# Optimization experiments

Measured on AMD Instinct MI355X. Metric: run time of the kernel, lower is better.

The kernel has to match this reference:

```python
import jax, jax.numpy as jnp
import numpy as np
from jax import lax

D_MODEL = 64
D_STATE = 16
D_INNER = 128   # expand * d_model
DT_RANK = 4     # ceil(d_model / 16)
D_CONV = 4      # mamba_ssm default causal conv width
N_MAMBA = 6


def _gelu(x):
    return jax.nn.gelu(x, approximate=False)


def _conv2d(x, w, b, groups=1):
    ph, pw = w.shape[2] // 2, w.shape[3] // 2
    y = lax.conv_general_dilated(x, w, (1, 1), [(ph, ph), (pw, pw)],
                                 dimension_numbers=('NCHW', 'OIHW', 'NCHW'),
                                 feature_group_count=groups)
    return y + b[None, :, None, None]


def _group_norm(x, w, b, groups=4, eps=1e-5):
    B, C, H, W = x.shape
    xr = x.reshape(B, groups, C // groups, H * W)
    m = xr.mean((2, 3), keepdims=True)
    v = ((xr - m) ** 2).mean((2, 3), keepdims=True)
    xr = (xr - m) * lax.rsqrt(v + eps)
    return xr.reshape(B, C, H, W) * w[None, :, None, None] + b[None, :, None, None]


def _res_conv(x, p):
    c1w, c1b, g1w, g1b, c2w, c2b, g2w, g2b = p
    h = _gelu(_group_norm(_conv2d(x, c1w, c1b), g1w, g1b))
    h = _group_norm(_conv2d(h, c2w, c2b), g2w, g2b)
    return _gelu(x + h)


def _mamba(u, in_w, conv_w, conv_b, xproj_w, dt_w, dt_b, A_log, Dp, out_w):
    # u: (B, L, d_model). Standard Mamba-1 selective scan via parallel assoc scan.
    x, z = jnp.split(u @ in_w.T, 2, axis=-1)            # (B,L,Di) each
    # causal depthwise conv1d, kernel D_CONV
    xt = lax.conv_general_dilated(x.transpose(0, 2, 1), conv_w[:, None, :], (1,),
                                  [(D_CONV - 1, 0)],
                                  dimension_numbers=('NCH', 'OIH', 'NCH'),
                                  feature_group_count=D_INNER)
    x = jax.nn.silu((xt + conv_b[None, :, None]).transpose(0, 2, 1))
    dt, Bc, Cc = jnp.split(x @ xproj_w.T, [DT_RANK, DT_RANK + D_STATE], axis=-1)
    dt = jax.nn.softplus(dt @ dt_w.T + dt_b)            # (B,L,Di)
    A = -jnp.exp(A_log)                                  # (Di,N)
    dA = jnp.exp(dt[..., None] * A)                      # (B,L,Di,N)
    dBx = dt[..., None] * Bc[:, :, None, :] * x[..., None]

    def comb(e1, e2):  # h_t = a_t*h_{t-1} + b_t
        a1, b1 = e1
        a2, b2 = e2
        return a1 * a2, b1 * a2 + b2

    _, h = lax.associative_scan(comb, (dA, dBx), axis=1)  # (B,L,Di,N)
    y = jnp.einsum('blds,bls->bld', h, Cc) + Dp * x
    y = y * jax.nn.silu(z)
    return y @ out_w.T


def _bi_mamba(u, mp, i_fwd, i_bwd):
    f = _mamba(u, *[p[i_fwd] for p in mp])
    b = jnp.flip(_mamba(jnp.flip(u, 1), *[p[i_bwd] for p in mp]), 1)
    return 0.5 * (f + b)


def _forward(x, m_in_w, m_conv_w, m_conv_b, m_xproj_w, m_dt_w, m_dt_b, m_A_log,
             m_D, m_out_w, r1_c1_w, r1_c1_b, r1_g1_w, r1_g1_b, r1_c2_w, r1_c2_b,
             r1_g2_w, r1_g2_b, dw_w, dw_b, pw_w, pw_b, r2_c1_w, r2_c1_b, r2_g1_w,
             r2_g1_b, r2_c2_w, r2_c2_b, r2_g2_w, r2_g2_b):
    B, D, H, W = x.shape
    mp = (m_in_w, m_conv_w, m_conv_b, m_xproj_w, m_dt_w, m_dt_b, m_A_log, m_D, m_out_w)
    x_flat = x.reshape(B, D, H * W).transpose(0, 2, 1)   # (B, HW, D)
    # spatial bidirectional mamba
    x_spatial = _bi_mamba(x_flat, mp, 0, 1).transpose(0, 2, 1).reshape(B, D, H, W)
    # local conv branch
    xl = _res_conv(x_spatial, (r1_c1_w, r1_c1_b, r1_g1_w, r1_g1_b, r1_c2_w, r1_c2_b, r1_g2_w, r1_g2_b))
    xl = _gelu(_conv2d(xl, dw_w, dw_b, groups=D))
    xl = _conv2d(xl, pw_w, pw_b)
    xl = _res_conv(xl, (r2_c1_w, r2_c1_b, r2_g1_w, r2_g1_b, r2_c2_w, r2_c2_b, r2_g2_w, r2_g2_b))
    # 'time' branch on original input (same flattening as x_flat)
    x_tg = _bi_mamba(x_flat, mp, 2, 3).transpose(0, 2, 1).reshape(B, D, H, W)
    # downsampled branch
    x_ds = x.reshape(B, D, H // 2, 2, W // 2, 2).mean((3, 5))
    ds_flat = x_ds.reshape(B, D, (H // 2) * (W // 2)).transpose(0, 2, 1)
    x_td = _bi_mamba(ds_flat, mp, 4, 5).transpose(0, 2, 1).reshape(B, D, H // 2, W // 2)
    x_td = jax.image.resize(x_td, (B, D, H, W), method='bilinear')
    return x_spatial + xl + 0.5 * x_tg + 0.5 * x_td


def setup_inputs() -> dict:
    key = jax.random.key(0)
    ks = iter(jax.random.split(key, 64))

    def rn(shape, s=0.02):
        return (s * jax.random.normal(next(ks), shape)).astype(jnp.float32)

    D, Di, N, R = D_MODEL, D_INNER, D_STATE, DT_RANK
    inp = {
        'x': jax.random.normal(next(ks), (2, D, 64, 64), dtype=jnp.float32),
        'm_in_w': rn((N_MAMBA, 2 * Di, D)),
        'm_conv_w': rn((N_MAMBA, Di, D_CONV), 0.1),
        'm_conv_b': rn((N_MAMBA, Di), 0.1),
        'm_xproj_w': rn((N_MAMBA, R + 2 * N, Di)),
        'm_dt_w': rn((N_MAMBA, Di, R), 0.1),
        'm_dt_b': rn((N_MAMBA, Di), 0.5),
        'm_A_log': jnp.tile(jnp.log(jnp.arange(1, N + 1, dtype=jnp.float32)), (N_MAMBA, Di, 1)),
        'm_D': jnp.ones((N_MAMBA, Di), jnp.float32),
        'm_out_w': rn((N_MAMBA, D, Di)),
        'dw_w': rn((D, 1, 3, 3), 0.1), 'dw_b': rn((D,), 0.1),
        'pw_w': rn((D, D, 1, 1), 0.05), 'pw_b': rn((D,), 0.1),
    }
    for pre in ('r1', 'r2'):
        inp[pre + '_c1_w'] = rn((D, D, 3, 3), 0.05)
        inp[pre + '_c1_b'] = rn((D,), 0.1)
        inp[pre + '_g1_w'] = jnp.ones((D,), jnp.float32)
        inp[pre + '_g1_b'] = jnp.zeros((D,), jnp.float32)
        inp[pre + '_c2_w'] = rn((D, D, 3, 3), 0.05)
        inp[pre + '_c2_b'] = rn((D,), 0.1)
        inp[pre + '_g2_w'] = jnp.ones((D,), jnp.float32)
        inp[pre + '_g2_b'] = jnp.zeros((D,), jnp.float32)
    return inp


def reference(x, m_in_w, m_conv_w, m_conv_b, m_xproj_w, m_dt_w, m_dt_b, m_A_log,
              m_D, m_out_w, r1_c1_w, r1_c1_b, r1_g1_w, r1_g1_b, r1_c2_w, r1_c2_b,
              r1_g2_w, r1_g2_b, dw_w, dw_b, pw_w, pw_b, r2_c1_w, r2_c1_b, r2_g1_w,
              r2_g1_b, r2_c2_w, r2_c2_b, r2_g2_w, r2_g2_b):
    return _forward(x, m_in_w, m_conv_w, m_conv_b, m_xproj_w, m_dt_w, m_dt_b,
                    m_A_log, m_D, m_out_w, r1_c1_w, r1_c1_b, r1_g1_w, r1_g1_b,
                    r1_c2_w, r1_c2_b, r1_g2_w, r1_g2_b, dw_w, dw_b, pw_w, pw_b,
                    r2_c1_w, r2_c1_b, r2_g1_w, r2_g1_b, r2_c2_w, r2_c2_b,
                    r2_g2_w, r2_g2_b)
```

## Files before the change

kernel.cpp:

```cpp
#include <hip/hip_runtime.h>
#include <hip/hip_bf16.h>

typedef __hip_bfloat16 bf16;
typedef unsigned short u16;
typedef unsigned int u32;
typedef __attribute__((ext_vector_type(8))) short short8v;
typedef __attribute__((ext_vector_type(4))) float f32x4;


#define XCB_OFF   0u
#define DTB_OFF   2359296u
#define BCB_OFF   4718592u
#define CHA_OFF   5308416u
#define CHH_OFF   7667712u
#define XZ_OFF    10027008u
#define UFS_OFF   14745600u
#define UFD_OFF   15269888u
#define XS_OFF    15400960u
#define XTG_OFF   15925248u
#define XTD_OFF   16449536u
#define XSB_OFF   16580608u
#define WT4_OFF   16842752u
#define STATS_OFF 16916480u
#define FLAG_OFF  16916736u
#define PRM_OFF   16916752u
#define PART_OFF  17091184u
#define CV0_OFF   0u
#define CV1_OFF   524288u
#define A1B_OFF   1048576u
#define A2B_OFF   1310720u
#define PWB_OFF   1572864u

__device__ __forceinline__ float bits2f(u16 v){
  u32 u = ((u32)v) << 16; float f; __builtin_memcpy(&f, &u, 4); return f;
}
__device__ __forceinline__ float b2f(bf16 v){ return __bfloat162float(v); }
__device__ __forceinline__ u16 f2bu(float f){ bf16 h = __float2bfloat16(f); u16 b; __builtin_memcpy(&b, &h, 2); return b; }
__device__ __forceinline__ float silu_f(float x){ return x / (1.f + __expf(-x)); }
__device__ __forceinline__ float softplus_f(float x){ return fmaxf(x, 0.f) + log1pf(__expf(-fabsf(x))); }
__device__ __forceinline__ float gelu_f(float x){ return 0.5f * x * (1.f + erff(x * 0.70710678118654752f)); }
__device__ __forceinline__ short8v zero8(){ short8v z = {0,0,0,0,0,0,0,0}; return z; }
__device__ __forceinline__ void up2(u32 w, float& a, float& b){
  a = bits2f((u16)(w & 0xffffu)); b = bits2f((u16)(w >> 16));
}
__device__ __forceinline__ void powchain(float r, float* aa){
  aa[0]=r; aa[1]=r*r; aa[2]=aa[1]*r; aa[3]=aa[1]*aa[1];
  aa[4]=aa[3]*r; aa[5]=aa[3]*aa[1]; aa[6]=aa[3]*aa[2]; aa[7]=aa[3]*aa[3];
  aa[8]=aa[7]*r; aa[9]=aa[7]*aa[1]; aa[10]=aa[7]*aa[2]; aa[11]=aa[7]*aa[3];
  aa[12]=aa[7]*aa[4]; aa[13]=aa[7]*aa[5]; aa[14]=aa[7]*aa[6]; aa[15]=aa[7]*aa[7];
}

struct P29 { const void* p[29]; };

__constant__ int PREF[30] = {0, 98304, 101376, 102144, 129792, 132864, 133632,
  145920, 146688, 195840, 196416, 196480, 200576, 200640, 237504, 237568,
  237632, 237696, 274560, 274624, 274688, 274752, 311616, 311680, 311744,
  311808, 348672, 348736, 348800, 348864};

__constant__ float LOGT[16] = {0.0f, 0.6931472f, 1.0986123f, 1.3862944f,
  1.6094379f, 1.7917595f, 1.9459101f, 2.0794415f, 2.1972246f, 2.3025851f,
  2.3978953f, 2.4849067f, 2.5649493f, 2.6390573f, 2.7080502f, 2.7725887f};

__global__ void k_detect(const void* __restrict__ xraw, const void* __restrict__ araw,
                         float* __restrict__ ws){
  __shared__ int cnt_s, bad_s;
  int tid = threadIdx.x;
  if (tid == 0){ cnt_s = 0; bad_s = 0; }
  __syncthreads();
  const u16* p = (const u16*)xraw;
  int c = 0;
  for (int i = tid; i < 4096; i += 256){
    int e = (p[i] >> 7) & 0xFF;
    if (e >= 0x77 && e <= 0x87) c++;
  }
  atomicAdd(&cnt_s, c);
  __syncthreads();
  int flag = (cnt_s > 3500) ? 0 : 1;
  int bad = 0;
  for (int i = tid; i < 12288; i += 256){
    float v = flag ? ((const float*)araw)[i] : b2f(((const bf16*)araw)[i]);
    if (fabsf(v - LOGT[i & 15]) > 0.02f) bad = 1;
  }
  if (bad) atomicAdd(&bad_s, 1);
  __syncthreads();
  if (tid == 0){
    ((int*)(ws + FLAG_OFF))[0] = flag;
    ((int*)(ws + FLAG_OFF))[1] = (bad_s == 0) ? 1 : 0;
  }
}

__global__ __launch_bounds__(256) void k_setup(P29 ptrs, const void* __restrict__ xraw,
                                               float* __restrict__ ws){
  int bid = blockIdx.x, tid = threadIdx.x;
  int flag = *(const int*)(ws + FLAG_OFF);
  const float* xf = (const float*)xraw;
  const bf16*  xb = (const bf16*)xraw;
  if (bid < 2560){
    int i = bid * 256 + tid;
    if (i < 524288){
      int b = i >> 18, rem = i & 262143, l = rem >> 6, d = rem & 63;
      size_t idx = (size_t)b*262144 + d*4096 + l;
      ws[UFS_OFF + i] = flag ? xf[idx] : b2f(xb[idx]);
    } else if (i < 655360){
      int j = i - 524288;
      int b = j >> 16, rem = j & 65535, l = rem >> 6, d = rem & 63;
      int i2 = l >> 5, j2 = l & 31;
      size_t base = (size_t)b*262144 + d*4096 + (i2*2)*64 + j2*2;
      float v0, v1, v2, v3;
      if (flag){ v0 = xf[base]; v1 = xf[base+1]; v2 = xf[base+64]; v3 = xf[base+65]; }
      else     { v0 = b2f(xb[base]); v1 = b2f(xb[base+1]); v2 = b2f(xb[base+64]); v3 = b2f(xb[base+65]); }
      ws[UFD_OFF + j] = 0.25f * (v0 + v1 + v2 + v3);
    }
  } else if (bid < 3923){
    int i = (bid - 2560) * 256 + tid;
    if (i < 348864){
      int t = 0;
      #pragma unroll 1
      while (i >= PREF[t + 1]) ++t;
      int off = i - PREF[t];
      float v = flag ? ((const float*)ptrs.p[t])[off]
                     : b2f(((const bf16*)ptrs.p[t])[off]);
      ((bf16*)(ws + PRM_OFF))[i] = __float2bfloat16(v);
    }
  } else {
    int i = (bid - 3923) * 256 + tid;
    if (i < 147456){
      int conv = i / 36864, r = i - conv * 36864;
      int tap = r >> 12, co = (r >> 6) & 63, ci = r & 63;
      const int SRC[4] = {13, 17, 21, 25};
      const void* sp_ = ptrs.p[SRC[conv]];
      size_t off = (size_t)co * 576 + ci * 9 + tap;
      float v = flag ? ((const float*)sp_)[off] : b2f(((const bf16*)sp_)[off]);
      ((bf16*)(ws + WT4_OFF))[i] = __float2bfloat16(v);
    }
  }
}

__device__ __forceinline__ void chunk_map(int bid, int& g, int& c0){
  if (bid < 1024){ g = bid >> 7; c0 = bid & 127; }
  else { int r = bid - 1024; g = 8 + (r >> 5); c0 = r & 31; }
}

__global__ __launch_bounds__(256) void k_inproj(const float* __restrict__ ws,
        bf16* __restrict__ XZ, const bf16* __restrict__ in_w){
  __shared__ __align__(16) u16 u_s[32][72];
  int g, tile; chunk_map(blockIdx.x, g, tile);
  int dir = (g < 8) ? (g >> 1) : 4 + ((g - 8) >> 1);
  int b   = (g < 8) ? (g & 1) : ((g - 8) & 1);
  int rev = dir & 1;
  int L   = (g < 8) ? 4096 : 1024;
  int row0 = (g < 8) ? g * 4096 : 32768 + (g - 8) * 1024;
  int t0 = tile * 32;
  const float* U = (g < 8) ? (ws + UFS_OFF + (size_t)b * 262144)
                           : (ws + UFD_OFF + (size_t)b * 65536);
  int tid = threadIdx.x;
  for (int e = tid; e < 2048; e += 256){
    int i = e >> 6, d = e & 63;
    int l = rev ? (L - 1 - (t0 + i)) : (t0 + i);
    u_s[i][d] = f2bu(U[(size_t)l * 64 + d]);
  }
  __syncthreads();
  int w = tid >> 6, lane = tid & 63;
  int l15 = lane & 15, ko = lane >> 4;
  short8v Au[2][2];
  #pragma unroll
  for (int mt = 0; mt < 2; ++mt)
    #pragma unroll
    for (int kk = 0; kk < 2; ++kk)
      Au[mt][kk] = *(const short8v*)&u_s[mt * 16 + l15][kk * 32 + ko * 8];
  const u16* wg = (const u16*)in_w + (size_t)dir * 16384;
  u16* XZu = (u16*)XZ;
  #pragma unroll
  for (int nq = 0; nq < 4; ++nq){
    int nt = w * 4 + nq;
    int c = nt * 16 + l15;
    short8v B0 = *(const short8v*)(wg + (size_t)c * 64 + ko * 8);
    short8v B1 = *(const short8v*)(wg + (size_t)c * 64 + 32 + ko * 8);
    #pragma unroll
    for (int mt = 0; mt < 2; ++mt){
      f32x4 acc = {0.f, 0.f, 0.f, 0.f};
      acc = __builtin_amdgcn_mfma_f32_16x16x32_bf16(Au[mt][0], B0, acc, 0, 0, 0);
      acc = __builtin_amdgcn_mfma_f32_16x16x32_bf16(Au[mt][1], B1, acc, 0, 0, 0);
      #pragma unroll
      for (int reg = 0; reg < 4; ++reg){
        int t = t0 + mt * 16 + ko * 4 + reg;
        XZu[(size_t)(row0 + t) * 256 + c] = f2bu(acc[reg]);
      }
    }
  }
}

__global__ __launch_bounds__(256) void k_front(float* __restrict__ ws,
        const bf16* __restrict__ xproj_w, const bf16* __restrict__ dt_w, const bf16* __restrict__ dt_b,
        const bf16* __restrict__ conv_w, const bf16* __restrict__ conv_b, const bf16* __restrict__ A_log){
  __shared__ __align__(16) u32 xstage[2310];
  __shared__ __align__(16) u16 xc_s[32][136];
  __shared__ __align__(16) u32 blob[4352];
  float* xp_s = (float*)xstage;
  u16* xw_s = (u16*)blob;
  float* cmb = (float*)blob;

  int g, c0; chunk_map(blockIdx.x, g, c0);
  int dir = (g < 8) ? (g >> 1) : 4 + ((g - 8) >> 1);
  int grow0 = (g < 8) ? g * 4096 : 32768 + (g - 8) * 1024;
  int t0 = c0 << 5;
  int crow = ((g < 8) ? g * 128 : 1024 + (g - 8) * 32) + c0;
  int tid = threadIdx.x;

  const u32* XZ32 = (const u32*)(ws + XZ_OFF);
  for (int e = tid; e < 2240; e += 256){
    int lr = e >> 6, col = e & 63;
    int gt = t0 - 3 + lr;
    u32 v = 0u;
    if (gt >= 0) v = XZ32[(size_t)(grow0 + gt) * 128 + col];
    xstage[lr * 66 + col] = v;
  }
  const u16* xw = (const u16*)xproj_w + (size_t)dir * 4608;
  for (int e = tid; e < 6144; e += 256){
    int m = e >> 7, col = e & 127;
    xw_s[m * 136 + col] = (m < 36) ? xw[m * 128 + col] : (u16)0;
  }
  __syncthreads();

  int c = tid & 127, hf = tid >> 7;
  int rb = hf * 16;
  {
    const u16* cwp = (const u16*)conv_w + (size_t)dir * 512 + c * 4;
    uint2 cw2 = *(const uint2*)cwp;
    float cw0, cw1, cw2f, cw3;
    up2(cw2.x, cw0, cw1); up2(cw2.y, cw2f, cw3);
    float cb = b2f(conv_b[dir * 128 + c]);
    const u16* xsu = (const u16*)xstage;
    float xm3 = bits2f(xsu[rb * 132 + c]);
    float xm2 = bits2f(xsu[(rb + 1) * 132 + c]);
    float xm1 = bits2f(xsu[(rb + 2) * 132 + c]);
    u16* XCBu = (u16*)(ws + XCB_OFF);
    #pragma unroll 4
    for (int t = 0; t < 16; ++t){
      float xcur = bits2f(xsu[(rb + t + 3) * 132 + c]);
      float s = cb + cw0 * xm3 + cw1 * xm2 + cw2f * xm1 + cw3 * xcur;
      u16 xbv = f2bu(silu_f(s));
      xm3 = xm2; xm2 = xm1; xm1 = xcur;
      xc_s[rb + t][c] = xbv;
      XCBu[(size_t)(grow0 + t0 + rb + t) * 128 + c] = xbv;
    }
  }
  __syncthreads();

  {
    int w = tid >> 6, lane = tid & 63;
    int l15 = lane & 15, ko = lane >> 4;
    for (int task = w; task < 6; task += 4){
      int mt = task & 1, nt = task >> 1;
      f32x4 acc = {0.f, 0.f, 0.f, 0.f};
      #pragma unroll
      for (int kk = 0; kk < 4; ++kk){
        short8v Afr = *(const short8v*)&xc_s[mt * 16 + l15][kk * 32 + ko * 8];
        short8v Bfr = *(const short8v*)(xw_s + (size_t)(nt * 16 + l15) * 136 + kk * 32 + ko * 8);
        acc = __builtin_amdgcn_mfma_f32_16x16x32_bf16(Afr, Bfr, acc, 0, 0, 0);
      }
      int j = nt * 16 + l15;
      if (j < 36){
        #pragma unroll
        for (int reg = 0; reg < 4; ++reg){
          int t = mt * 16 + ko * 4 + reg;
          xp_s[t * 40 + j] = acc[reg];
        }
      }
    }
  }
  __syncthreads();

  {
    u16* BCBu = (u16*)(ws + BCB_OFF);
    for (int e = tid; e < 1024; e += 256){
      int t = e >> 5, v = e & 31;
      float val = xp_s[t * 40 + 4 + v];
      u16 r = f2bu(val);
      xp_s[t * 40 + 4 + v] = bits2f(r);
      BCBu[(size_t)(grow0 + t0 + t) * 32 + v] = r;
    }
  }
  __syncthreads();

  {
    int apat = ((const int*)(ws + FLAG_OFF))[1];
    float A[16];
    const u16* ap = (const u16*)A_log + (size_t)dir * 2048 + c * 16;
    #pragma unroll
    for (int s = 0; s < 16; ++s) A[s] = -__expf(bits2f(ap[s]));
    const u16* dwp = (const u16*)dt_w + (size_t)dir * 512 + c * 4;
    uint2 dw2 = *(const uint2*)dwp;
    float d0, d1, d2, d3;
    up2(dw2.x, d0, d1); up2(dw2.y, d2, d3);
    float db = b2f(dt_b[dir * 128 + c]);
    u16* DTBu = (u16*)(ws + DTB_OFF);
    float hh[16], p[16];
    #pragma unroll
    for (int s = 0; s < 16; ++s){ hh[s] = 0.f; p[s] = 1.f; }
    float dtsum = 0.f;
    #pragma unroll 2
    for (int t = 0; t < 16; ++t){
      float4 xp4 = *(const float4*)&xp_s[(rb + t) * 40];
      float dtv = softplus_f(db + d0 * xp4.x + d1 * xp4.y + d2 * xp4.z + d3 * xp4.w);
      u16 dtb16 = f2bu(dtv);
      DTBu[(size_t)(grow0 + t0 + rb + t) * 128 + c] = dtb16;
      float dtu = bits2f(dtb16);
      float xcv = bits2f(xc_s[rb + t][c]);
      float dx = dtu * xcv;
      float aa[16];
      if (apat){
        dtsum += dtu;
        powchain(__expf(-dtu), aa);
      } else {
        #pragma unroll
        for (int s = 0; s < 16; ++s) aa[s] = __expf(dtu * A[s]);
        #pragma unroll
        for (int s = 0; s < 16; ++s) p[s] *= aa[s];
      }
      #pragma unroll
      for (int s = 0; s < 16; ++s)
        hh[s] = fmaf(aa[s], hh[s], dx * xp_s[(rb + t) * 40 + 4 + s]);
    }
    if (apat) powchain(__expf(-dtsum), p);
    if (hf == 0){
      #pragma unroll
      for (int s = 0; s < 16; ++s){
        cmb[c * 17 + s] = p[s];
        cmb[2176 + c * 17 + s] = hh[s];
      }
    }
    __syncthreads();
    if (hf == 1){
      float ca[16], ch[16];
      #pragma unroll
      for (int s = 0; s < 16; ++s){
        float P0 = cmb[c * 17 + s];
        float H0 = cmb[2176 + c * 17 + s];
        ca[s] = P0 * p[s];
        ch[s] = fmaf(p[s], H0, hh[s]);
      }
      float* CA = ws + CHA_OFF + (size_t)crow * 2048 + c * 16;
      float* CH = ws + CHH_OFF + (size_t)crow * 2048 + c * 16;
      #pragma unroll
      for (int q = 0; q < 4; ++q){
        *(float4*)(CA + q * 4) = make_float4(ca[q*4], ca[q*4+1], ca[q*4+2], ca[q*4+3]);
        *(float4*)(CH + q * 4) = make_float4(ch[q*4], ch[q*4+1], ch[q*4+2], ch[q*4+3]);
      }
    }
  }
}

__global__ __launch_bounds__(256) void k_scan2(float* __restrict__ ws){
  int id = blockIdx.x * 256 + threadIdx.x;
  int gi = id >> 11, dsl = id & 2047;
  int nc = (gi < 8) ? 128 : 32;
  int cb = (gi < 8) ? gi * 128 : 1024 + (gi - 8) * 32;
  float* CA = ws + CHA_OFF; float* CH = ws + CHH_OFF;
  float hprev = 0.f;
  for (int ch = 0; ch < nc; ch += 8){
    size_t i0 = (size_t)(cb + ch) * 2048 + dsl;
    float a[8], hv[8];
    #pragma unroll
    for (int j = 0; j < 8; ++j){
      a[j] = CA[i0 + (size_t)j * 2048];
      hv[j] = CH[i0 + (size_t)j * 2048];
    }
    #pragma unroll
    for (int j = 0; j < 8; ++j){
      CH[i0 + (size_t)j * 2048] = hprev;
      hprev = fmaf(a[j], hprev, hv[j]);
    }
  }
}

__global__ __launch_bounds__(256) void k_outproj(float* __restrict__ ws, const bf16* __restrict__ out_w,
        const bf16* __restrict__ A_log, const bf16* __restrict__ Dp){
  __shared__ __align__(16) u16 yf_s[32][132];
  __shared__ __align__(16) u16 yb_s[32][132];
  int bid = blockIdx.x;
  int pair, b, tile, L;
  if (bid < 512){ pair = bid >> 8; b = (bid >> 7) & 1; tile = bid & 127; L = 4096; }
  else { int r = bid - 512; pair = 2; b = r >> 5; tile = r & 31; L = 1024; }
  int l0 = tile * 32;
  int ncht = L >> 5;
  int df = pair * 2, db_ = df + 1;
  int gf = (pair < 2) ? df * 2 + b : 8 + b;
  int gb = (pair < 2) ? db_ * 2 + b : 10 + b;
  int rowf0 = (gf < 8) ? gf * 4096 : 32768 + (gf - 8) * 1024;
  int rowb0 = (gb < 8) ? gb * 4096 : 32768 + (gb - 8) * 1024;
  int tid = threadIdx.x;

  {
    int half = tid >> 7, d = tid & 127;
    int gS = half ? gb : gf;
    int dirS = (gS < 8) ? (gS >> 1) : 4 + ((gS - 8) >> 1);
    int rowS = half ? (rowb0 + (L - 32 - l0)) : (rowf0 + l0);
    int cbaseS = (gS < 8) ? gS * 128 : 1024 + (gS - 8) * 32;
    int crowS = cbaseS + (half ? (ncht - 1 - tile) : tile);
    int apat = ((const int*)(ws + FLAG_OFF))[1];
    float A[16];
    const u16* ap = (const u16*)A_log + (size_t)dirS * 2048 + d * 16;
    #pragma unroll
    for (int s = 0; s < 16; ++s) A[s] = -__expf(bits2f(ap[s]));
    float h[16];
    const float* CH = ws + CHH_OFF + (size_t)crowS * 2048 + d * 16;
    #pragma unroll
    for (int s = 0; s < 16; ++s) h[s] = CH[s];
    float Dv = b2f(Dp[dirS * 128 + d]);
    const u16* XCBu = (const u16*)(ws + XCB_OFF);
    const u16* DTBu = (const u16*)(ws + DTB_OFF);
    const u16* BCBu = (const u16*)(ws + BCB_OFF);
    const u16* XZu  = (const u16*)(ws + XZ_OFF);
    #pragma unroll 2
    for (int t = 0; t < 32; ++t){
      size_t r = (size_t)(rowS + t);
      float dtu = bits2f(DTBu[r * 128 + d]);
      float xcv = bits2f(XCBu[r * 128 + d]);
      float zv  = bits2f(XZu[r * 256 + 128 + d]);
      const uint4* bp = (const uint4*)(BCBu + r * 32);
      uint4 q0 = bp[0], q1 = bp[1], q2 = bp[2], q3 = bp[3];
      float Bv[16], Cv[16];
      up2(q0.x, Bv[0], Bv[1]);  up2(q0.y, Bv[2], Bv[3]);  up2(q0.z, Bv[4], Bv[5]);  up2(q0.w, Bv[6], Bv[7]);
      up2(q1.x, Bv[8], Bv[9]);  up2(q1.y, Bv[10], Bv[11]); up2(q1.z, Bv[12], Bv[13]); up2(q1.w, Bv[14], Bv[15]);
      up2(q2.x, Cv[0], Cv[1]);  up2(q2.y, Cv[2], Cv[3]);  up2(q2.z, Cv[4], Cv[5]);  up2(q2.w, Cv[6], Cv[7]);
      up2(q3.x, Cv[8], Cv[9]);  up2(q3.y, Cv[10], Cv[11]); up2(q3.z, Cv[12], Cv[13]); up2(q3.w, Cv[14], Cv[15]);
      float dx = dtu * xcv;
      float aa[16];
      if (apat){
        powchain(__expf(-dtu), aa);
      } else {
        #pragma unroll
        for (int s = 0; s < 16; ++s) aa[s] = __expf(dtu * A[s]);
      }
      float y = 0.f;
      #pragma unroll
      for (int s = 0; s < 16; ++s){
        h[s] = fmaf(aa[s], h[s], dx * Bv[s]);
        y = fmaf(h[s], Cv[s], y);
      }
      y = fmaf(Dv, xcv, y);
      u16 yv = f2bu(y * silu_f(zv));
      if (half == 0) yf_s[t][d] = yv;
      else           yb_s[31 - t][d] = yv;
    }
  }
  __syncthreads();

  int w = tid >> 6, lane = tid & 63;
  int l15 = lane & 15, ko = lane >> 4;
  int mt = w & 1, nh = w >> 1;
  const u16* wf = (const u16*)out_w + (size_t)df * 8192;
  const u16* wb = (const u16*)out_w + (size_t)db_ * 8192;
  short8v Af[4], Ab[4];
  #pragma unroll
  for (int kk = 0; kk < 4; ++kk){
    Af[kk] = *(const short8v*)&yf_s[mt * 16 + l15][kk * 32 + ko * 8];
    Ab[kk] = *(const short8v*)&yb_s[mt * 16 + l15][kk * 32 + ko * 8];
  }
  float* xo = ws + ((pair == 0) ? XS_OFF : (pair == 1) ? XTG_OFF : XTD_OFF);
  int Lout = (pair < 2) ? 4096 : 1024;
  u16* xsb = (u16*)(ws + XSB_OFF);
  #pragma unroll
  for (int ct = 0; ct < 2; ++ct){
    int c = nh * 32 + ct * 16 + l15;
    f32x4 acc = {0.f, 0.f, 0.f, 0.f};
    #pragma unroll
    for (int kk = 0; kk < 4; ++kk){
      short8v Bf = *(const short8v*)(wf + (size_t)c * 128 + kk * 32 + ko * 8);
      acc = __builtin_amdgcn_mfma_f32_16x16x32_bf16(Af[kk], Bf, acc, 0, 0, 0);
      short8v Bb = *(const short8v*)(wb + (size_t)c * 128 + kk * 32 + ko * 8);
      acc = __builtin_amdgcn_mfma_f32_16x16x32_bf16(Ab[kk], Bb, acc, 0, 0, 0);
    }
    #pragma unroll
    for (int reg = 0; reg < 4; ++reg){
      int row = l0 + mt * 16 + ko * 4 + reg;
      float v = 0.5f * acc[reg];
      xo[((size_t)b * Lout + row) * 64 + c] = v;
      if (pair == 0) xsb[((size_t)b * 4096 + row) * 64 + c] = f2bu(v);
    }
  }
}

template<int NTAP>
__global__ __launch_bounds__(256) void k_convmfma(const bf16* __restrict__ act,
        float* __restrict__ outf, bf16* __restrict__ outb,
        const bf16* __restrict__ wt, const bf16* __restrict__ bias,
        float* __restrict__ part){
  __shared__ float red[4][4];
  int wid = blockIdx.x * 4 + (threadIdx.x >> 6);
  int lane = threadIdx.x & 63;
  int nc = wid & 1;
  int pt = wid >> 1;
  int b = pt >> 8, py = (pt >> 2) & 63, x0 = (pt & 3) << 4;
  int l15 = lane & 15, ko = lane >> 4;
  f32x4 acc0 = {0.f, 0.f, 0.f, 0.f}, acc1 = {0.f, 0.f, 0.f, 0.f};
  const bf16* ab = act + ((size_t)b * 4096) * 64;
  #pragma unroll
  for (int tap = 0; tap < NTAP; ++tap){
    int dy = (NTAP == 9) ? (tap / 3 - 1) : 0;
    int dx = (NTAP == 9) ? (tap % 3 - 1) : 0;
    int y = py + dy;
    bool yok = (NTAP == 1) || ((unsigned)y < 64u);
    int xx = x0 + l15 + dx;
    bool vall = yok && ((NTAP == 1) || ((unsigned)xx < 64u));
    const bf16* arow = ab + ((size_t)(y * 64 + xx)) * 64;
    const bf16* wrow = wt + (size_t)tap * 4096;
    #pragma unroll
    for (int kk = 0; kk < 2; ++kk){
      int ci0 = kk * 32 + ko * 8;
      short8v a;
      if (vall) a = *(const short8v*)(arow + ci0); else a = zero8();
      short8v bw0 = *(const short8v*)(wrow + (size_t)(nc * 32 + l15) * 64 + ci0);
      short8v bw1 = *(const short8v*)(wrow + (size_t)(nc * 32 + 16 + l15) * 64 + ci0);
      acc0 = __builtin_amdgcn_mfma_f32_16x16x32_bf16(a, bw0, acc0, 0, 0, 0);
      acc1 = __builtin_amdgcn_mfma_f32_16x16x32_bf16(a, bw1, acc1, 0, 0, 0);
    }
  }
  float bs0 = b2f(bias[nc * 32 + l15]);
  float bs1 = b2f(bias[nc * 32 + 16 + l15]);
  float s1a = 0.f, s2a = 0.f, s1b = 0.f, s2b = 0.f;
  size_t obase = ((size_t)b * 4096 + py * 64 + x0 + (ko << 2)) * 64 + nc * 32;
  #pragma unroll
  for (int r = 0; r < 4; ++r){
    float v0 = acc0[r] + bs0, v1 = acc1[r] + bs1;
    s1a += v0; s2a += v0 * v0; s1b += v1; s2b += v1 * v1;
    if (outf){
      outf[obase + (size_t)r * 64 + l15] = v0;
      outf[obase + (size_t)r * 64 + 16 + l15] = v1;
    } else {
      outb[obase + (size_t)r * 64 + l15] = __float2bfloat16(v0);
      outb[obase + (size_t)r * 64 + 16 + l15] = __float2bfloat16(v1);
    }
  }
  #pragma unroll
  for (int off = 1; off < 64; off <<= 1){
    s1a += __shfl_xor(s1a, off, 64); s2a += __shfl_xor(s2a, off, 64);
    s1b += __shfl_xor(s1b, off, 64); s2b += __shfl_xor(s2b, off, 64);
  }
  int w = threadIdx.x >> 6;
  if (lane == 0){ red[w][0] = s1a; red[w][1] = s2a; red[w][2] = s1b; red[w][3] = s2b; }
  __syncthreads();
  if (part && threadIdx.x < 8){
    int g = threadIdx.x >> 1, sel = threadIdx.x & 1;
    int w0 = g >> 1;
    int col = ((g & 1) << 1) + sel;
    part[(size_t)blockIdx.x * 8 + threadIdx.x] = red[w0][col] + red[w0 + 2][col];
  }
}

__global__ __launch_bounds__(256) void k_gn_act(const float* __restrict__ in, const float* __restrict__ res,
        bf16* __restrict__ outb, const float* __restrict__ part,
        const bf16* __restrict__ gw, const bf16* __restrict__ gb, int add_res){
  __shared__ float st8[8];
  int tid = threadIdx.x;
  int t = blockIdx.x * 256 + tid;
  int b = blockIdx.x >> 8;
  {
    int j = tid & 31, f = tid >> 5;
    float v = 0.f;
    #pragma unroll
    for (int k = 0; k < 4; ++k)
      v += part[(size_t)(b * 128 + j * 4 + k) * 8 + f];
    #pragma unroll
    for (int off = 16; off; off >>= 1) v += __shfl_down(v, off, 32);
    if (j == 0) st8[f] = v;
  }
  __syncthreads();
  int cq = t & 15, px = (t >> 4) & 4095;
  int c0 = cq * 4, g = cq >> 2;
  float mean = st8[g * 2] * (1.f / 65536.f);
  float rs = rsqrtf(st8[g * 2 + 1] * (1.f / 65536.f) - mean * mean + 1e-5f);
  size_t idx = ((size_t)b * 4096 + px) * 64 + c0;
  float4 f4 = *(const float4*)(in + idx);
  float vv[4] = {f4.x, f4.y, f4.z, f4.w};
  float rr[4] = {0.f, 0.f, 0.f, 0.f};
  if (add_res){ float4 r4 = *(const float4*)(res + idx); rr[0]=r4.x; rr[1]=r4.y; rr[2]=r4.z; rr[3]=r4.w; }
  u16 o[4];
  #pragma unroll
  for (int j = 0; j < 4; ++j){
    float v = (vv[j] - mean) * rs * b2f(gw[c0 + j]) + b2f(gb[c0 + j]);
    v += rr[j];
    o[j] = f2bu(gelu_f(v));
  }
  u32 lo = (u32)o[0] | ((u32)o[1] << 16);
  u32 hi = (u32)o[2] | ((u32)o[3] << 16);
  *(uint2*)((u16*)outb + idx) = make_uint2(lo, hi);
}

__global__ __launch_bounds__(256) void k_dwgelu(const bf16* __restrict__ in, bf16* __restrict__ out,
        const bf16* __restrict__ w, const bf16* __restrict__ bias){
  int id = blockIdx.x * 256 + threadIdx.x;
  int oc8 = id & 7, px = (id >> 3) & 4095, b = id >> 15;
  int py = px >> 6, pxx = px & 63;
  float wv[8][9];
  #pragma unroll
  for (int j = 0; j < 8; ++j)
    #pragma unroll
    for (int tp = 0; tp < 9; ++tp) wv[j][tp] = b2f(w[(oc8 * 8 + j) * 9 + tp]);
  float acc[8];
  #pragma unroll
  for (int j = 0; j < 8; ++j) acc[j] = b2f(bias[oc8 * 8 + j]);
  const bf16* inb = in + ((size_t)b * 4096) * 64;
  #pragma unroll
  for (int dy = 0; dy < 3; ++dy){
    int y = py + dy - 1;
    if ((unsigned)y >= 64u) continue;
    #pragma unroll
    for (int dx = 0; dx < 3; ++dx){
      int x = pxx + dx - 1;
      if ((unsigned)x >= 64u) continue;
      short8v iv = *(const short8v*)(inb + ((size_t)(y * 64 + x)) * 64 + oc8 * 8);
      #pragma unroll
      for (int j = 0; j < 8; ++j)
        acc[j] = fmaf(bits2f((u16)iv[j]), wv[j][dy * 3 + dx], acc[j]);
    }
  }
  u32 pk[4];
  #pragma unroll
  for (int k = 0; k < 4; ++k){
    u16 a0 = f2bu(gelu_f(acc[2 * k]));
    u16 a1 = f2bu(gelu_f(acc[2 * k + 1]));
    pk[k] = (u32)a0 | ((u32)a1 << 16);
  }
  *(uint4*)((u16*)out + ((size_t)b * 4096 + px) * 64 + oc8 * 8) = make_uint4(pk[0], pk[1], pk[2], pk[3]);
}

__global__ __launch_bounds__(256) void k_final(const float* __restrict__ ws, void* __restrict__ outp,
        const bf16* __restrict__ gw, const bf16* __restrict__ gb){
  __shared__ float st8[8];
  int flag = *(const int*)(ws + FLAG_OFF);
  int bid = blockIdx.x;
  int b = bid >> 6, py = bid & 63;
  int t = threadIdx.x;
  {
    const float* part = ws + PART_OFF + 3 * 2048;
    int j = t & 31, f = t >> 5;
    float v = 0.f;
    #pragma unroll
    for (int k = 0; k < 4; ++k)
      v += part[(size_t)(b * 128 + j * 4 + k) * 8 + f];
    #pragma unroll
    for (int off = 16; off; off >>= 1) v += __shfl_down(v, off, 32);
    if (j == 0) st8[f] = v;
  }
  __syncthreads();
  int c = t & 63, pxg = t >> 6;
  int g = c >> 4;
  float mean = st8[g * 2] * (1.f / 65536.f);
  float rs = rsqrtf(st8[g * 2 + 1] * (1.f / 65536.f) - mean * mean + 1e-5f);
  float gwv = b2f(gw[c]), gbv = b2f(gb[c]);
  const float* CV1 = ws + CV1_OFF;
  const bf16* PWB = (const bf16*)(ws + PWB_OFF);
  const float* XS = ws + XS_OFF;
  const float* XTG = ws + XTG_OFF;
  const float* XTD = ws + XTD_OFF + ((size_t)b * 1024) * 64;
  float sy = 0.5f * py - 0.25f;
  float fly = floorf(sy); float fy = sy - fly;
  int iy0 = max((int)fly, 0), iy1 = min((int)fly + 1, 31);
  float of[16];
  #pragma unroll
  for (int i = 0; i < 16; ++i){
    int px = pxg * 16 + i;
    size_t idx = ((size_t)b * 4096 + py * 64 + px) * 64 + c;
    float gn = (CV1[idx] - mean) * rs * gwv + gbv;
    float xl = gelu_f(b2f(PWB[idx]) + gn);
    float sx = 0.5f * px - 0.25f;
    float flx = floorf(sx); float fx = sx - flx;
    int ix0 = max((int)flx, 0), ix1 = min((int)flx + 1, 31);
    float v00 = XTD[(size_t)(iy0 * 32 + ix0) * 64 + c], v01 = XTD[(size_t)(iy0 * 32 + ix1) * 64 + c];
    float v10 = XTD[(size_t)(iy1 * 32 + ix0) * 64 + c], v11 = XTD[(size_t)(iy1 * 32 + ix1) * 64 + c];
    float tdv = (1.f - fy) * ((1.f - fx) * v00 + fx * v01) + fy * ((1.f - fx) * v10 + fx * v11);
    of[i] = XS[idx] + xl + 0.5f * XTG[idx] + 0.5f * tdv;
  }
  size_t ob = ((size_t)(b * 64 + c)) * 4096 + py * 64 + pxg * 16;
  if (flag){
    float* o = (float*)outp + ob;
    #pragma unroll
    for (int k = 0; k < 4; ++k)
      *(float4*)(o + k * 4) = make_float4(of[k*4], of[k*4+1], of[k*4+2], of[k*4+3]);
  } else {
    u16* o = (u16*)outp + ob;
    u32 pk[8];
    #pragma unroll
    for (int k = 0; k < 8; ++k)
      pk[k] = (u32)f2bu(of[2*k]) | ((u32)f2bu(of[2*k+1]) << 16);
    *(uint4*)(o) = make_uint4(pk[0], pk[1], pk[2], pk[3]);
    *(uint4*)(o + 8) = make_uint4(pk[4], pk[5], pk[6], pk[7]);
  }
}

extern "C" void kernel_launch(void* const* d_in, const int* in_sizes, int n_in,
                              void* d_out, int out_size, void* d_ws, size_t ws_size,
                              hipStream_t stream) {
  float* ws = (float*)d_ws;
  bf16* XZ = (bf16*)(ws + XZ_OFF);
  bf16* prm = (bf16*)(ws + PRM_OFF);
  bf16* WT4 = (bf16*)(ws + WT4_OFF);
  bf16* XSB = (bf16*)(ws + XSB_OFF);
  bf16* A1B = (bf16*)(ws + A1B_OFF);
  bf16* A2B = (bf16*)(ws + A2B_OFF);
  bf16* PWBb = (bf16*)(ws + PWB_OFF);
  float* CV0 = ws + CV0_OFF;
  float* CV1 = ws + CV1_OFF;
  float* PART = ws + PART_OFF;

  const bf16* m_in_w   = prm + 0;
  const bf16* m_conv_w = prm + 98304;
  const bf16* m_conv_b = prm + 101376;
  const bf16* m_xproj  = prm + 102144;
  const bf16* m_dt_w   = prm + 129792;
  const bf16* m_dt_b   = prm + 132864;
  const bf16* m_A_log  = prm + 133632;
  const bf16* m_D      = prm + 145920;
  const bf16* m_out_w  = prm + 146688;
  const bf16* dw_w  = prm + 195840;
  const bf16* dw_b  = prm + 196416;
  const bf16* pw_w  = prm + 196480;
  const bf16* pw_b  = prm + 200576;
  const bf16* r1c1b = prm + 237504;
  const bf16* r1g1w = prm + 237568;
  const bf16* r1g1b = prm + 237632;
  const bf16* r1c2b = prm + 274560;
  const bf16* r1g2w = prm + 274624;
  const bf16* r1g2b = prm + 274688;
  const bf16* r2c1b = prm + 311616;
  const bf16* r2g1w = prm + 311680;
  const bf16* r2g1b = prm + 311744;
  const bf16* r2c2b = prm + 348672;
  const bf16* r2g2w = prm + 348736;
  const bf16* r2g2b = prm + 348800;

  P29 ptrs;
  for (int t = 0; t < 29; ++t) ptrs.p[t] = d_in[t + 1];

  k_detect<<<1, 256, 0, stream>>>(d_in[0], d_in[7], ws);
  k_setup<<<4499, 256, 0, stream>>>(ptrs, d_in[0], ws);
  k_inproj<<<1152, 256, 0, stream>>>(ws, XZ, m_in_w);
  k_front<<<1152, 256, 0, stream>>>(ws, m_xproj, m_dt_w, m_dt_b, m_conv_w, m_conv_b, m_A_log);
  k_scan2<<<96, 256, 0, stream>>>(ws);
  k_outproj<<<576, 256, 0, stream>>>(ws, m_out_w, m_A_log, m_D);

  k_convmfma<9><<<256, 256, 0, stream>>>(XSB, CV0, (bf16*)nullptr, WT4 + 0 * 36864, r1c1b, PART + 0 * 2048);
  k_gn_act<<<512, 256, 0, stream>>>(CV0, (const float*)nullptr, A1B, PART + 0 * 2048, r1g1w, r1g1b, 0);
  k_convmfma<9><<<256, 256, 0, stream>>>(A1B, CV1, (bf16*)nullptr, WT4 + 1 * 36864, r1c2b, PART + 1 * 2048);
  k_gn_act<<<512, 256, 0, stream>>>(CV1, ws + XS_OFF, A2B, PART + 1 * 2048, r1g2w, r1g2b, 1);
  k_dwgelu<<<256, 256, 0, stream>>>(A2B, A1B, dw_w, dw_b);
  k_convmfma<1><<<256, 256, 0, stream>>>(A1B, (float*)nullptr, PWBb, pw_w, pw_b, (float*)nullptr);
  k_convmfma<9><<<256, 256, 0, stream>>>(PWBb, CV0, (bf16*)nullptr, WT4 + 2 * 36864, r2c1b, PART + 2 * 2048);
  k_gn_act<<<512, 256, 0, stream>>>(CV0, (const float*)nullptr, A1B, PART + 2 * 2048, r2g1w, r2g1b, 0);
  k_convmfma<9><<<256, 256, 0, stream>>>(A1B, CV1, (bf16*)nullptr, WT4 + 3 * 36864, r2c2b, PART + 3 * 2048);
  k_final<<<128, 256, 0, stream>>>(ws, d_out, r2g2w, r2g2b);
}
```

Baseline: 206.8 us.

## Fuse Mamba input projection into front kernel, recomputing conv halo rows

Merges the in_proj MFMA kernel into k_front so the x half of the projection stays in shared memory instead of being written to and re-read from global XZ. Only the z half is still stored globally. The three causal-conv halo rows before each 32-row chunk are recomputed per block with scalar FMAs from the input. This removes one kernel launch and a global round trip of the x activations, at the cost of redundant halo work, more shared memory per block and extra scalar FMAs.

```diff
diff --git a/kernel.cpp b/kernel.cpp
--- a/kernel.cpp
+++ b/kernel.cpp
@@ -141,84 +141,94 @@
   else { int r = bid - 1024; g = 8 + (r >> 5); c0 = r & 31; }
 }
 
-__global__ __launch_bounds__(256) void k_inproj(const float* __restrict__ ws,
-        bf16* __restrict__ XZ, const bf16* __restrict__ in_w){
-  __shared__ __align__(16) u16 u_s[32][72];
-  int g, tile; chunk_map(blockIdx.x, g, tile);
+__global__ __launch_bounds__(256) void k_front(float* __restrict__ ws, const bf16* __restrict__ in_w,
+        const bf16* __restrict__ xproj_w, const bf16* __restrict__ dt_w, const bf16* __restrict__ dt_b,
+        const bf16* __restrict__ conv_w, const bf16* __restrict__ conv_b, const bf16* __restrict__ A_log){
+  __shared__ __align__(16) u32 pool[1280];
+  __shared__ __align__(16) u16 x_s[35 * 132];
+  __shared__ __align__(16) u16 xc_s[32][136];
+  __shared__ __align__(16) u32 blob[4352];
+  u16* u_s = (u16*)pool;
+  float* xp_s = (float*)pool;
+  u16* xw_s = (u16*)blob;
+  float* cmb = (float*)blob;
+
+  int g, c0; chunk_map(blockIdx.x, g, c0);
   int dir = (g < 8) ? (g >> 1) : 4 + ((g - 8) >> 1);
-  int b   = (g < 8) ? (g & 1) : ((g - 8) & 1);
+  int bb  = (g < 8) ? (g & 1) : ((g - 8) & 1);
   int rev = dir & 1;
   int L   = (g < 8) ? 4096 : 1024;
-  int row0 = (g < 8) ? g * 4096 : 32768 + (g - 8) * 1024;
-  int t0 = tile * 32;
-  const float* U = (g < 8) ? (ws + UFS_OFF + (size_t)b * 262144)
-                           : (ws + UFD_OFF + (size_t)b * 65536);
-  int tid = threadIdx.x;
-  for (int e = tid; e < 2048; e += 256){
-    int i = e >> 6, d = e & 63;
-    int l = rev ? (L - 1 - (t0 + i)) : (t0 + i);
-    u_s[i][d] = f2bu(U[(size_t)l * 64 + d]);
-  }
-  __syncthreads();
-  int w = tid >> 6, lane = tid & 63;
-  int l15 = lane & 15, ko = lane >> 4;
-  short8v Au[2][2];
-  #pragma unroll
-  for (int mt = 0; mt < 2; ++mt)
-    #pragma unroll
-    for (int kk = 0; kk < 2; ++kk)
-      Au[mt][kk] = *(const short8v*)&u_s[mt * 16 + l15][kk * 32 + ko * 8];
-  const u16* wg = (const u16*)in_w + (size_t)dir * 16384;
-  u16* XZu = (u16*)XZ;
-  #pragma unroll
-  for (int nq = 0; nq < 4; ++nq){
-    int nt = w * 4 + nq;
-    int c = nt * 16 + l15;
-    short8v B0 = *(const short8v*)(wg + (size_t)c * 64 + ko * 8);
-    short8v B1 = *(const short8v*)(wg + (size_t)c * 64 + 32 + ko * 8);
-    #pragma unroll
-    for (int mt = 0; mt < 2; ++mt){
-      f32x4 acc = {0.f, 0.f, 0.f, 0.f};
-      acc = __builtin_amdgcn_mfma_f32_16x16x32_bf16(Au[mt][0], B0, acc, 0, 0, 0);
-      acc = __builtin_amdgcn_mfma_f32_16x16x32_bf16(Au[mt][1], B1, acc, 0, 0, 0);
-      #pragma unroll
-      for (int reg = 0; reg < 4; ++reg){
-        int t = t0 + mt * 16 + ko * 4 + reg;
-        XZu[(size_t)(row0 + t) * 256 + c] = f2bu(acc[reg]);
-      }
-    }
-  }
-}
-
-__global__ __launch_bounds__(256) void k_front(float* __restrict__ ws,
-        const bf16* __restrict__ xproj_w, const bf16* __restrict__ dt_w, const bf16* __restrict__ dt_b,
-        const bf16* __restrict__ conv_w, const bf16* __restrict__ conv_b, const bf16* __restrict__ A_log){
-  __shared__ __align__(16) u32 xstage[2310];
-  __shared__ __align__(16) u16 xc_s[32][136];
-  __shared__ __align__(16) u32 blob[4352];
-  float* xp_s = (float*)xstage;
-  u16* xw_s = (u16*)blob;
-  float* cmb = (float*)blob;
-
-  int g, c0; chunk_map(blockIdx.x, g, c0);
-  int dir = (g < 8) ? (g >> 1) : 4 + ((g - 8) >> 1);
   int grow0 = (g < 8) ? g * 4096 : 32768 + (g - 8) * 1024;
   int t0 = c0 << 5;
   int crow = ((g < 8) ? g * 128 : 1024 + (g - 8) * 32) + c0;
+  const float* U = (g < 8) ? (ws + UFS_OFF + (size_t)bb * 262144)
+                           : (ws + UFD_OFF + (size_t)bb * 65536);
   int tid = threadIdx.x;
 
-  const u32* XZ32 = (const u32*)(ws + XZ_OFF);
   for (int e = tid; e < 2240; e += 256){
-    int lr = e >> 6, col = e & 63;
+    int lr = e >> 6, k = e & 63;
     int gt = t0 - 3 + lr;
-    u32 v = 0u;
-    if (gt >= 0) v = XZ32[(size_t)(grow0 + gt) * 128 + col];
-    xstage[lr * 66 + col] = v;
+    float v = 0.f;
+    if (gt >= 0){
+      int l = rev ? (L - 1 - gt) : gt;
+      v = U[(size_t)l * 64 + k];
+    }
+    u_s[lr * 72 + k] = f2bu(v);
   }
   const u16* xw = (const u16*)xproj_w + (size_t)dir * 4608;
   for (int e = tid; e < 6144; e += 256){
     int m = e >> 7, col = e & 127;
     xw_s[m * 136 + col] = (m < 36) ? xw[m * 128 + col] : (u16)0;
+  }
+  __syncthreads();
+
+  {
+    int w = tid >> 6, lane = tid & 63;
+    int l15 = lane & 15, ko = lane >> 4;
+    short8v Au[2][2];
+    #pragma unroll
+    for (int mt = 0; mt < 2; ++mt)
+      #pragma unroll
+      for (int kk = 0; kk < 2; ++kk)
+        Au[mt][kk] = *(const short8v*)(u_s + (size_t)(3 + mt * 16 + l15) * 72 + kk * 32 + ko * 8);
+    const u16* wg = (const u16*)in_w + (size_t)dir * 16384;
+    u16* XZu = (u16*)(ws + XZ_OFF);
+    #pragma unroll
+    for (int nq = 0; nq < 4; ++nq){
+      int nt = w * 4 + nq;
+      int c = nt * 16 + l15;
+      short8v B0 = *(const short8v*)(wg + (size_t)c * 64 + ko * 8);
+      short8v B1 = *(const short8v*)(wg + (size_t)c * 64 + 32 + ko * 8);
+      #pragma unroll
+      for (int mt = 0; mt < 2; ++mt){
+        f32x4 acc = {0.f, 0.f, 0.f, 0.f};
+        acc = __builtin_amdgcn_mfma_f32_16x16x32_bf16(Au[mt][0], B0, acc, 0, 0, 0);
+        acc = __builtin_amdgcn_mfma_f32_16x16x32_bf16(Au[mt][1], B1, acc, 0, 0, 0);
+        #pragma unroll
+        for (int reg = 0; reg < 4; ++reg){
+          int t = mt * 16 + ko * 4 + reg;
+          u16 v = f2bu(acc[reg]);
+          if (c < 128) x_s[(3 + t) * 132 + c] = v;
+          else XZu[(size_t)(grow0 + t0 + t) * 256 + c] = v;
+        }
+      }
+    }
+    for (int task = tid; task < 384; task += 256){
+      int lr = task >> 7, cc = task & 127;
+      int gt = t0 - 3 + lr;
+      float acc = 0.f;
+      if (gt >= 0){
+        const u16* wr = wg + (size_t)cc * 64;
+        #pragma unroll
+        for (int j = 0; j < 8; ++j){
+          short8v wv = *(const short8v*)(wr + j * 8);
+          #pragma unroll
+          for (int q = 0; q < 8; ++q)
+            acc = fmaf(bits2f(u_s[lr * 72 + j * 8 + q]), bits2f((u16)wv[q]), acc);
+        }
+      }
+      x_s[lr * 132 + cc] = f2bu(acc);
+    }
   }
   __syncthreads();
 
@@ -230,14 +240,13 @@
     float cw0, cw1, cw2f, cw3;
     up2(cw2.x, cw0, cw1); up2(cw2.y, cw2f, cw3);
     float cb = b2f(conv_b[dir * 128 + c]);
-    const u16* xsu = (const u16*)xstage;
-    float xm3 = bits2f(xsu[rb * 132 + c]);
-    float xm2 = bits2f(xsu[(rb + 1) * 132 + c]);
-    float xm1 = bits2f(xsu[(rb + 2) * 132 + c]);
+    float xm3 = bits2f(x_s[rb * 132 + c]);
+    float xm2 = bits2f(x_s[(rb + 1) * 132 + c]);
+    float xm1 = bits2f(x_s[(rb + 2) * 132 + c]);
     u16* XCBu = (u16*)(ws + XCB_OFF);
     #pragma unroll 4
     for (int t = 0; t < 16; ++t){
-      float xcur = bits2f(xsu[(rb + t + 3) * 132 + c]);
+      float xcur = bits2f(x_s[(rb + t + 3) * 132 + c]);
       float s = cb + cw0 * xm3 + cw1 * xm2 + cw2f * xm1 + cw3 * xcur;
       u16 xbv = f2bu(silu_f(s));
       xm3 = xm2; xm2 = xm1; xm1 = xcur;
@@ -694,7 +703,6 @@
                               void* d_out, int out_size, void* d_ws, size_t ws_size,
                               hipStream_t stream) {
   float* ws = (float*)d_ws;
-  bf16* XZ = (bf16*)(ws + XZ_OFF);
   bf16* prm = (bf16*)(ws + PRM_OFF);
   bf16* WT4 = (bf16*)(ws + WT4_OFF);
   bf16* XSB = (bf16*)(ws + XSB_OFF);
@@ -736,8 +744,7 @@
 
   k_detect<<<1, 256, 0, stream>>>(d_in[0], d_in[7], ws);
   k_setup<<<4499, 256, 0, stream>>>(ptrs, d_in[0], ws);
-  k_inproj<<<1152, 256, 0, stream>>>(ws, XZ, m_in_w);
-  k_front<<<1152, 256, 0, stream>>>(ws, m_xproj, m_dt_w, m_dt_b, m_conv_w, m_conv_b, m_A_log);
+  k_front<<<1152, 256, 0, stream>>>(ws, m_in_w, m_xproj, m_dt_w, m_dt_b, m_conv_w, m_conv_b, m_A_log);
   k_scan2<<<96, 256, 0, stream>>>(ws);
   k_outproj<<<576, 256, 0, stream>>>(ws, m_out_w, m_A_log, m_D);
 
```

Measured after the change: 208.2 us. No clear change (+0.7%).
